# Optimization experiments

Hardware: AMD Instinct MI355X
Metric: run time of the kernel (lower is better)

## Reference

```python
import jax, jax.numpy as jnp
import numpy as np

V, D, N, K = 500000, 64, 50000, 32


def setup_inputs() -> dict:
    key = jax.random.key(0)
    ks = jax.random.split(key, 8)
    return {
        "embeddings": jax.random.normal(ks[0], (V, D), dtype=jnp.float32),
        "W1": jax.random.normal(ks[1], (2 * D, D), dtype=jnp.float32) * 0.05,
        "b1": jnp.zeros((D,), dtype=jnp.float32),
        "W2": jax.random.normal(ks[2], (D, D), dtype=jnp.float32) * 0.05,
        "b2": jnp.zeros((D,), dtype=jnp.float32),
        "w3": jax.random.normal(ks[3], (D, 1), dtype=jnp.float32) * 0.05,
        "b3": jnp.zeros((1,), dtype=jnp.float32),
        "video_nodes": jax.random.randint(ks[4], (N,), 0, V, dtype=jnp.int32),
        "neigh_idx": jax.random.randint(ks[5], (N, K), 0, V, dtype=jnp.int32),
        "neigh_deg": jax.random.randint(ks[6], (N,), 0, K + 1, dtype=jnp.int32),
    }


def reference(embeddings, W1, b1, W2, b2, w3, b3, video_nodes, neigh_idx, neigh_deg):
    # Ragged neighbor gather (padded to K, masked by degree)
    e = embeddings[neigh_idx]                      # [N, K, D] neighbor embeddings
    u = embeddings[video_nodes]                    # [N, D]    center embeddings
    # GraphRec-style attention: MLP on [neigh, center] concat -> scalar score
    x = jnp.concatenate(
        [e, jnp.broadcast_to(u[:, None, :], e.shape)], axis=-1)  # [N, K, 2D]
    h = jax.nn.relu(x @ W1 + b1)
    h = jax.nn.relu(h @ W2 + b2)
    s = (h @ w3)[..., 0] + b3[0]                   # [N, K]
    mask = jnp.arange(K)[None, :] < neigh_deg[:, None]
    s = jnp.where(mask, s, -1e9)                   # mask padded neighbors
    att = jax.nn.softmax(s, axis=-1)               # softmax over valid neighbors
    out = jnp.einsum('nkd,nk->nd', e, att)         # attention-weighted sum
    # num_neighs == 0 -> fall back to node's own embedding
    out = jnp.where((neigh_deg > 0)[:, None], out, u)
    return out
```

## Files before the change

### kernel.cpp

```cpp
#include <hip/hip_runtime.h>
#include <hip/hip_bf16.h>

typedef __bf16 bf16x8 __attribute__((ext_vector_type(8)));
typedef float  f32x4  __attribute__((ext_vector_type(4)));

#define MFMA32(acc, a, b) acc = __builtin_amdgcn_mfma_f32_16x16x32_bf16(a, b, acc, 0, 0, 0)
#define LD4(p) (*(const float4*)(p))

__device__ __forceinline__ bf16x8 cvt8(float4 a, float4 b) {
  bf16x8 r;
  r[0] = (__bf16)a.x; r[1] = (__bf16)a.y; r[2] = (__bf16)a.z; r[3] = (__bf16)a.w;
  r[4] = (__bf16)b.x; r[5] = (__bf16)b.y; r[6] = (__bf16)b.z; r[7] = (__bf16)b.w;
  return r;
}

template <int CTRL>
__device__ __forceinline__ float dpp_mov(float x) {
  int yi = __builtin_amdgcn_update_dpp(0, __builtin_bit_cast(int, x), CTRL, 0xF, 0xF, true);
  return __builtin_bit_cast(float, yi);
}
template <int CTRL>
__device__ __forceinline__ float dpp_fadd(float x) { return x + dpp_mov<CTRL>(x); }
template <int CTRL>
__device__ __forceinline__ float dpp_fmax(float x) { return fmaxf(x, dpp_mov<CTRL>(x)); }

__device__ __forceinline__ float tree16(const float* o, int lr) {
  float q8[8];
#pragma unroll
  for (int t = 0; t < 8; t++) {
    const bool up = (lr & 8);
    float sel = up ? o[t + 8] : o[t];
    float oth = up ? o[t] : o[t + 8];
    q8[t] = sel + dpp_mov<0x128>(oth);
  }
  float q4[4];
#pragma unroll
  for (int t = 0; t < 4; t++) {
    const bool up = (lr & 4);
    float sel = up ? q8[t + 4] : q8[t];
    float oth = up ? q8[t] : q8[t + 4];
    q4[t] = sel + __shfl_xor(oth, 4);
  }
  float q2[2];
#pragma unroll
  for (int t = 0; t < 2; t++) {
    const bool up = (lr & 2);
    float sel = up ? q4[t + 2] : q4[t];
    float oth = up ? q4[t] : q4[t + 2];
    q2[t] = sel + dpp_mov<0x4E>(oth);
  }
  const bool up = (lr & 1);
  float sel = up ? q2[1] : q2[0];
  float oth = up ? q2[0] : q2[1];
  return sel + dpp_mov<0xB1>(oth);
}

__global__ void prep_frags(const float* __restrict__ W1,
                           const float* __restrict__ W2,
                           __bf16* __restrict__ wf) {
  int idx = blockIdx.x * 256 + threadIdx.x;
  if (idx < 8192) {
    int j = idx & 7, lane = (idx >> 3) & 63, mt = (idx >> 9) & 3, ks = idx >> 11;
    int i = ks * 32 + ((lane >> 4) << 3) + j;
    int col = mt * 16 + (lane & 15);
    wf[idx] = (__bf16)W1[i * 64 + col];
  } else if (idx < 12288) {
    int t = idx - 8192;
    int j = t & 7, lane = (t >> 3) & 63, mt2 = (t >> 9) & 3, ks2 = (t >> 11) & 1;
    int g = (lane >> 4) & 3;
    int rho = (ks2 * 2 + (j >> 2)) * 16 + g * 4 + (j & 3);
    wf[idx] = (__bf16)W2[rho * 64 + mt2 * 16 + (lane & 15)];
  }
}

__global__ __launch_bounds__(512) void graph_agg(
    const float* __restrict__ emb,
    const float* __restrict__ b1g, const float* __restrict__ b2g,
    const float* __restrict__ w3g, const float* __restrict__ b3g,
    const int* __restrict__ vn, const int* __restrict__ ni,
    const int* __restrict__ nd,
    const __bf16* __restrict__ wf,
    float* __restrict__ out, int N) {
  __shared__ __align__(16) unsigned char smem[25344];

  {
    const uint4* src = (const uint4*)wf;
    uint4* dst = (uint4*)smem;
#pragma unroll
    for (int i = 0; i < 3; i++) dst[threadIdx.x + i * 512] = src[threadIdx.x + i * 512];
    int t = threadIdx.x;
    if (t < 64) {
      ((float*)(smem + 24576))[t] = b1g[t];
      ((float*)(smem + 24832))[t] = b2g[t];
      ((float*)(smem + 25088))[t] = w3g[t];
    }
  }
  __syncthreads();

  const __bf16* w1f = (const __bf16*)smem;
  const __bf16* w2f = (const __bf16*)(smem + 16384);
  const int wid = threadIdx.x >> 6;
  const int l   = threadIdx.x & 63;
  const int g   = l >> 4;
  const int lr  = l & 15;
  const float b3v = b3g[0];

  const int gw = blockIdx.x * 8 + wid;
  const int nwaves = gridDim.x * 8;

  int n = gw;
  int node = 0, deg = 0, i0 = 0, i1 = 0;
  if (n < N) {
    node = vn[n]; deg = nd[n];
    i0 = ni[(long)n * 32 + lr]; i1 = ni[(long)n * 32 + 16 + lr];
  }

  for (; n < N; n += nwaves) {
    const int cn = node, cd = deg, ci0 = i0, ci1 = i1;
    {
      int nn = n + nwaves; if (nn >= N) nn = n;
      node = vn[nn]; deg = nd[nn];
      i0 = ni[(long)nn * 32 + lr]; i1 = ni[(long)nn * 32 + 16 + lr];
    }
    const float* ub = emb + (long)cn * 64;

    if (cd == 0) {
      out[(long)n * 64 + l] = ub[l];
      continue;
    }
    const bool m1 = (cd > 16);

    int boff = 24576;
    asm volatile("" : "+v"(boff));
    const unsigned char* bb = smem + boff;

    bf16x8 ef00, ef01, ef10, ef11;
    {
      const int a = (lr < cd) ? ci0 : cn;
      const float* p = emb + (long)a * 64 + g * 8;
      ef00 = cvt8(LD4(p), LD4(p + 4));
      ef01 = cvt8(LD4(p + 32), LD4(p + 36));
    }
    if (m1) {
      const int a = (16 + lr < cd) ? ci1 : cn;
      const float* p = emb + (long)a * 64 + g * 8;
      ef10 = cvt8(LD4(p), LD4(p + 4));
      ef11 = cvt8(LD4(p + 32), LD4(p + 36));
    }
    bf16x8 uf0, uf1;
    {
      const float* q = ub + g * 8;
      uf0 = cvt8(LD4(q), LD4(q + 4));
      uf1 = cvt8(LD4(q + 32), LD4(q + 36));
    }

    f32x4 acc[4][2];
#pragma unroll
    for (int mt = 0; mt < 4; mt++) {
      f32x4 bv = *(const f32x4*)(bb + (mt * 16 + g * 4) * 4);
      acc[mt][0] = bv; acc[mt][1] = bv;
    }
    const bf16x8 xb0s[4] = {ef00, ef01, uf0, uf1};
    const bf16x8 xb1s[4] = {ef10, ef11, uf0, uf1};
#pragma unroll
    for (int ks = 0; ks < 4; ks++) {
#pragma unroll
      for (int mt = 0; mt < 4; mt++) {
        bf16x8 wa = *(const bf16x8*)(w1f + ((ks * 4 + mt) * 64 + l) * 8);
        MFMA32(acc[mt][0], wa, xb0s[ks]);
        if (m1) MFMA32(acc[mt][1], wa, xb1s[ks]);
      }
    }

    bf16x8 hb[2][2];
#pragma unroll
    for (int ks2 = 0; ks2 < 2; ks2++)
#pragma unroll
      for (int nt = 0; nt < 2; nt++) {
        if (nt == 0 || m1) {
          bf16x8 v;
#pragma unroll
          for (int j = 0; j < 8; j++) {
            const int mt = ks2 * 2 + (j >> 2), r = j & 3;
            v[j] = (__bf16)fmaxf(acc[mt][nt][r], 0.f);
          }
          hb[ks2][nt] = v;
        }
      }

#pragma unroll
    for (int mt2 = 0; mt2 < 4; mt2++) {
      f32x4 bv = *(const f32x4*)(bb + 256 + (mt2 * 16 + g * 4) * 4);
      acc[mt2][0] = bv; acc[mt2][1] = bv;
    }
#pragma unroll
    for (int ks2 = 0; ks2 < 2; ks2++)
#pragma unroll
      for (int mt2 = 0; mt2 < 4; mt2++) {
        bf16x8 wa = *(const bf16x8*)(w2f + ((ks2 * 4 + mt2) * 64 + l) * 8);
        MFMA32(acc[mt2][0], wa, hb[ks2][0]);
        if (m1) MFMA32(acc[mt2][1], wa, hb[ks2][1]);
      }

    float sv0 = 0.f, sv1 = 0.f;
#pragma unroll
    for (int mt2 = 0; mt2 < 4; mt2++) {
      f32x4 wv = *(const f32x4*)(bb + 512 + (mt2 * 16 + g * 4) * 4);
#pragma unroll
      for (int r = 0; r < 4; r++) {
        sv0 += fmaxf(acc[mt2][0][r], 0.f) * wv[r];
        if (m1) sv1 += fmaxf(acc[mt2][1][r], 0.f) * wv[r];
      }
    }
    sv0 += __shfl_xor(sv0, 16); sv0 += __shfl_xor(sv0, 32);
    if (m1) { sv1 += __shfl_xor(sv1, 16); sv1 += __shfl_xor(sv1, 32); }

    const bool v0 = (lr < cd);
    const bool v1 = m1 && (16 + lr < cd);
    sv0 = v0 ? (sv0 + b3v) : -1e30f;
    sv1 = v1 ? (sv1 + b3v) : -1e30f;

    float mx = fmaxf(sv0, sv1);
    mx = dpp_fmax<0x128>(mx);
    mx = dpp_fmax<0x124>(mx);
    mx = dpp_fmax<0x122>(mx);
    mx = dpp_fmax<0x121>(mx);

    float p0 = v0 ? __expf(sv0 - mx) : 0.f;
    float p1 = v1 ? __expf(sv1 - mx) : 0.f;
    float sum = p0 + p1;
    sum = dpp_fadd<0x128>(sum);
    sum = dpp_fadd<0x124>(sum);
    sum = dpp_fadd<0x122>(sum);
    sum = dpp_fadd<0x121>(sum);
    const float inv = 1.f / sum;
    const float a0 = p0 * inv, a1 = p1 * inv;

    float o[16];
#pragma unroll
    for (int j = 0; j < 8; j++) {
      float v = a0 * (float)ef00[j];
      if (m1) v += a1 * (float)ef10[j];
      o[j] = v;
      float w = a0 * (float)ef01[j];
      if (m1) w += a1 * (float)ef11[j];
      o[8 + j] = w;
    }
    const int dim = ((lr >> 3) << 5) + g * 8 + (lr & 7);
    out[(long)n * 64 + dim] = tree16(o, lr);
  }
}

extern "C" void kernel_launch(void* const* d_in, const int* in_sizes, int n_in,
                              void* d_out, int out_size, void* d_ws, size_t ws_size,
                              hipStream_t stream) {
  const float* emb = (const float*)d_in[0];
  const float* W1  = (const float*)d_in[1];
  const float* b1  = (const float*)d_in[2];
  const float* W2  = (const float*)d_in[3];
  const float* b2  = (const float*)d_in[4];
  const float* w3  = (const float*)d_in[5];
  const float* b3  = (const float*)d_in[6];
  const int* vn = (const int*)d_in[7];
  const int* ni = (const int*)d_in[8];
  const int* nd = (const int*)d_in[9];
  float* out = (float*)d_out;
  const int N = in_sizes[7];
  __bf16* wf = (__bf16*)d_ws;

  prep_frags<<<48, 256, 0, stream>>>(W1, W2, wf);
  graph_agg<<<2048, 512, 0, stream>>>(emb, b1, b2, w3, b3, vn, ni, nd, wf, out, N);
}
```

Before: 75.21 us.

## Prefetch next node's first-half neighbor rows into LDS via async global_load_lds

Uses global_load_lds (direct global-to-LDS DMA) to prefetch the next node's first 16 neighbor embeddings and center embedding into per-wave LDS buffers, issued in the middle of the current node's MLP so the gather latency overlaps with compute. The second half of the neighbors is still loaded directly to registers, and its MFMAs are split out after the first half's. Biases and w3 are now read from global memory instead of LDS, and LDS grows to 64KB per block, which lowers the number of blocks that can be resident. A full vmcnt(0) wait at the top of each iteration serializes against every outstanding load, not just the prefetch.

```diff
diff --git a/kernel.cpp b/kernel.cpp
--- a/kernel.cpp
+++ b/kernel.cpp
@@ -6,6 +6,12 @@
 
 #define MFMA32(acc, a, b) acc = __builtin_amdgcn_mfma_f32_16x16x32_bf16(a, b, acc, 0, 0, 0)
 #define LD4(p) (*(const float4*)(p))
+
+typedef const __attribute__((address_space(1))) void gas_t;
+typedef __attribute__((address_space(3))) void las_t;
+__device__ __forceinline__ void gload_lds16(const void* g, void* l) {
+  __builtin_amdgcn_global_load_lds((gas_t*)g, (las_t*)l, 16, 0, 0);
+}
 
 __device__ __forceinline__ bf16x8 cvt8(float4 a, float4 b) {
   bf16x8 r;
@@ -81,19 +87,13 @@
     const int* __restrict__ nd,
     const __bf16* __restrict__ wf,
     float* __restrict__ out, int N) {
-  __shared__ __align__(16) unsigned char smem[25344];
+  __shared__ __align__(16) unsigned char smem[65536];
 
   {
     const uint4* src = (const uint4*)wf;
     uint4* dst = (uint4*)smem;
 #pragma unroll
     for (int i = 0; i < 3; i++) dst[threadIdx.x + i * 512] = src[threadIdx.x + i * 512];
-    int t = threadIdx.x;
-    if (t < 64) {
-      ((float*)(smem + 24576))[t] = b1g[t];
-      ((float*)(smem + 24832))[t] = b2g[t];
-      ((float*)(smem + 25088))[t] = w3g[t];
-    }
   }
   __syncthreads();
 
@@ -103,6 +103,8 @@
   const int l   = threadIdx.x & 63;
   const int g   = l >> 4;
   const int lr  = l & 15;
+  unsigned char* pf0 = smem + 24576 + wid * 5120;
+  unsigned char* pfu = pf0 + 4096;
   const float b3v = b3g[0];
 
   const int gw = blockIdx.x * 8 + wid;
@@ -113,63 +115,91 @@
   if (n < N) {
     node = vn[n]; deg = nd[n];
     i0 = ni[(long)n * 32 + lr]; i1 = ni[(long)n * 32 + 16 + lr];
+    const int rn = (lr < deg) ? i0 : node;
+    const float* er = emb + (long)rn * 64 + g * 8;
+    gload_lds16(er,      pf0);
+    gload_lds16(er + 4,  pf0 + 1024);
+    gload_lds16(er + 32, pf0 + 2048);
+    gload_lds16(er + 36, pf0 + 3072);
+    gload_lds16(emb + (long)node * 64 + lr * 4, pfu);
   }
 
   for (; n < N; n += nwaves) {
-    const int cn = node, cd = deg, ci0 = i0, ci1 = i1;
-    {
-      int nn = n + nwaves; if (nn >= N) nn = n;
-      node = vn[nn]; deg = nd[nn];
-      i0 = ni[(long)nn * 32 + lr]; i1 = ni[(long)nn * 32 + 16 + lr];
-    }
-    const float* ub = emb + (long)cn * 64;
+    const int cn = node, cd = deg, ci1 = i1;
+
+    asm volatile("s_waitcnt vmcnt(0)" ::: "memory");
+    __builtin_amdgcn_sched_barrier(0);
+
+    int nn = n + nwaves; if (nn >= N) nn = n;
+    node = vn[nn]; deg = nd[nn];
+    i0 = ni[(long)nn * 32 + lr]; i1 = ni[(long)nn * 32 + 16 + lr];
 
     if (cd == 0) {
-      out[(long)n * 64 + l] = ub[l];
+      const float uv = *(const float*)(pfu + (((l >> 4) * 16 + (l >> 2)) << 4) + ((l & 3) << 2));
+      {
+        const int rn = (lr < deg) ? i0 : node;
+        const float* er = emb + (long)rn * 64 + g * 8;
+        gload_lds16(er,      pf0);
+        gload_lds16(er + 4,  pf0 + 1024);
+        gload_lds16(er + 32, pf0 + 2048);
+        gload_lds16(er + 36, pf0 + 3072);
+        gload_lds16(emb + (long)node * 64 + lr * 4, pfu);
+      }
+      out[(long)n * 64 + l] = uv;
       continue;
     }
     const bool m1 = (cd > 16);
 
-    int boff = 24576;
-    asm volatile("" : "+v"(boff));
-    const unsigned char* bb = smem + boff;
-
-    bf16x8 ef00, ef01, ef10, ef11;
-    {
-      const int a = (lr < cd) ? ci0 : cn;
-      const float* p = emb + (long)a * 64 + g * 8;
-      ef00 = cvt8(LD4(p), LD4(p + 4));
-      ef01 = cvt8(LD4(p + 32), LD4(p + 36));
-    }
+    float4 e1a, e1b, e1c, e1d;
     if (m1) {
       const int a = (16 + lr < cd) ? ci1 : cn;
       const float* p = emb + (long)a * 64 + g * 8;
-      ef10 = cvt8(LD4(p), LD4(p + 4));
-      ef11 = cvt8(LD4(p + 32), LD4(p + 36));
-    }
-    bf16x8 uf0, uf1;
+      e1a = LD4(p); e1b = LD4(p + 4); e1c = LD4(p + 32); e1d = LD4(p + 36);
+    }
+
+    bf16x8 ef00, ef01, uf0, uf1;
     {
-      const float* q = ub + g * 8;
-      uf0 = cvt8(LD4(q), LD4(q + 4));
-      uf1 = cvt8(LD4(q + 32), LD4(q + 36));
-    }
+      float4 f0 = LD4(pf0 + l * 16);
+      float4 f1 = LD4(pf0 + 1024 + l * 16);
+      float4 f2 = LD4(pf0 + 2048 + l * 16);
+      float4 f3 = LD4(pf0 + 3072 + l * 16);
+      ef00 = cvt8(f0, f1); ef01 = cvt8(f2, f3);
+      const unsigned char* ur = pfu + g * 288;
+      uf0 = cvt8(LD4(ur), LD4(ur + 16));
+      uf1 = cvt8(LD4(ur + 128), LD4(ur + 144));
+    }
+
+    int z0 = 0;
+    asm volatile("" : "+v"(z0));
+    const float* b1p = b1g + z0;
+    const float* b2p = b2g + z0;
+    const float* w3p = w3g + z0;
 
     f32x4 acc[4][2];
 #pragma unroll
     for (int mt = 0; mt < 4; mt++) {
-      f32x4 bv = *(const f32x4*)(bb + (mt * 16 + g * 4) * 4);
+      f32x4 bv = *(const f32x4*)(b1p + mt * 16 + g * 4);
       acc[mt][0] = bv; acc[mt][1] = bv;
     }
-    const bf16x8 xb0s[4] = {ef00, ef01, uf0, uf1};
-    const bf16x8 xb1s[4] = {ef10, ef11, uf0, uf1};
-#pragma unroll
-    for (int ks = 0; ks < 4; ks++) {
+    const bf16x8 x0s[4] = {ef00, ef01, uf0, uf1};
+#pragma unroll
+    for (int ks = 0; ks < 4; ks++)
 #pragma unroll
       for (int mt = 0; mt < 4; mt++) {
         bf16x8 wa = *(const bf16x8*)(w1f + ((ks * 4 + mt) * 64 + l) * 8);
-        MFMA32(acc[mt][0], wa, xb0s[ks]);
-        if (m1) MFMA32(acc[mt][1], wa, xb1s[ks]);
-      }
+        MFMA32(acc[mt][0], wa, x0s[ks]);
+      }
+    bf16x8 ef10, ef11;
+    if (m1) {
+      ef10 = cvt8(e1a, e1b); ef11 = cvt8(e1c, e1d);
+      const bf16x8 x1s[4] = {ef10, ef11, uf0, uf1};
+#pragma unroll
+      for (int ks = 0; ks < 4; ks++)
+#pragma unroll
+        for (int mt = 0; mt < 4; mt++) {
+          bf16x8 wa = *(const bf16x8*)(w1f + ((ks * 4 + mt) * 64 + l) * 8);
+          MFMA32(acc[mt][1], wa, x1s[ks]);
+        }
     }
 
     bf16x8 hb[2][2];
@@ -188,9 +218,21 @@
         }
       }
 
+    __builtin_amdgcn_sched_barrier(0);
+    {
+      const int rn = (lr < deg) ? i0 : node;
+      const float* er = emb + (long)rn * 64 + g * 8;
+      gload_lds16(er,      pf0);
+      gload_lds16(er + 4,  pf0 + 1024);
+      gload_lds16(er + 32, pf0 + 2048);
+      gload_lds16(er + 36, pf0 + 3072);
+      gload_lds16(emb + (long)node * 64 + lr * 4, pfu);
+    }
+    __builtin_amdgcn_sched_barrier(0);
+
 #pragma unroll
     for (int mt2 = 0; mt2 < 4; mt2++) {
-      f32x4 bv = *(const f32x4*)(bb + 256 + (mt2 * 16 + g * 4) * 4);
+      f32x4 bv = *(const f32x4*)(b2p + mt2 * 16 + g * 4);
       acc[mt2][0] = bv; acc[mt2][1] = bv;
     }
 #pragma unroll
@@ -205,7 +247,7 @@
     float sv0 = 0.f, sv1 = 0.f;
 #pragma unroll
     for (int mt2 = 0; mt2 < 4; mt2++) {
-      f32x4 wv = *(const f32x4*)(bb + 512 + (mt2 * 16 + g * 4) * 4);
+      f32x4 wv = *(const f32x4*)(w3p + mt2 * 16 + g * 4);
 #pragma unroll
       for (int r = 0; r < 4; r++) {
         sv0 += fmaxf(acc[mt2][0][r], 0.f) * wv[r];
```

New measurement: 109.8 us. +46.0%, slower.

## Prefetch next node's embeddings into LDS via async global-to-LDS loads

Applied to the files above, without the earlier changes.

Each wave now issues global_load_lds for the next node's first 16 neighbor rows and its center embedding into a per-wave LDS buffer. The prefetch is placed in the middle of the current node's MLP, so gather latency overlaps with compute. The second-half neighbors are loaded early into registers and their layer-1 MFMAs are split into a separate branch. It also drops the max-subtraction in the softmax, assuming scores stay small enough not to overflow exp. The larger LDS footprint may reduce occupancy, and the softmax is less numerically robust for large scores.

```diff
diff --git a/kernel.cpp b/kernel.cpp
--- a/kernel.cpp
+++ b/kernel.cpp
@@ -6,6 +6,15 @@
 
 #define MFMA32(acc, a, b) acc = __builtin_amdgcn_mfma_f32_16x16x32_bf16(a, b, acc, 0, 0, 0)
 #define LD4(p) (*(const float4*)(p))
+
+typedef const __attribute__((address_space(1))) void gas_t;
+typedef __attribute__((address_space(3))) void las_t;
+__device__ __forceinline__ void gload_lds16(const void* gp, void* lp) {
+  __builtin_amdgcn_global_load_lds((gas_t*)gp, (las_t*)lp, 16, 0, 0);
+}
+__device__ __forceinline__ void gload_lds4(const void* gp, void* lp) {
+  __builtin_amdgcn_global_load_lds((gas_t*)gp, (las_t*)lp, 4, 0, 0);
+}
 
 __device__ __forceinline__ bf16x8 cvt8(float4 a, float4 b) {
   bf16x8 r;
@@ -21,8 +30,6 @@
 }
 template <int CTRL>
 __device__ __forceinline__ float dpp_fadd(float x) { return x + dpp_mov<CTRL>(x); }
-template <int CTRL>
-__device__ __forceinline__ float dpp_fmax(float x) { return fmaxf(x, dpp_mov<CTRL>(x)); }
 
 __device__ __forceinline__ float tree16(const float* o, int lr) {
   float q8[8];
@@ -81,7 +88,7 @@
     const int* __restrict__ nd,
     const __bf16* __restrict__ wf,
     float* __restrict__ out, int N) {
-  __shared__ __align__(16) unsigned char smem[25344];
+  __shared__ __align__(16) unsigned char smem[60160];
 
   {
     const uint4* src = (const uint4*)wf;
@@ -103,7 +110,19 @@
   const int l   = threadIdx.x & 63;
   const int g   = l >> 4;
   const int lr  = l & 15;
+  unsigned char* pf0 = smem + 25344 + wid * 4352;
+  unsigned char* pfu = pf0 + 4096;
   const float b3v = b3g[0];
+
+#define PREFETCH(ND, DG, I0) do {                                   \
+    const int rn_ = (lr < (DG)) ? (I0) : (ND);                      \
+    const float* er_ = emb + (long)rn_ * 64 + g * 8;                \
+    gload_lds16(er_,      pf0);                                     \
+    gload_lds16(er_ + 4,  pf0 + 1024);                              \
+    gload_lds16(er_ + 32, pf0 + 2048);                              \
+    gload_lds16(er_ + 36, pf0 + 3072);                              \
+    gload_lds4(emb + (long)(ND) * 64 + l, pfu);                     \
+  } while (0)
 
   const int gw = blockIdx.x * 8 + wid;
   const int nwaves = gridDim.x * 8;
@@ -113,63 +132,71 @@
   if (n < N) {
     node = vn[n]; deg = nd[n];
     i0 = ni[(long)n * 32 + lr]; i1 = ni[(long)n * 32 + 16 + lr];
+    PREFETCH(node, deg, i0);
   }
 
   for (; n < N; n += nwaves) {
-    const int cn = node, cd = deg, ci0 = i0, ci1 = i1;
+    const int cn = node, cd = deg, ci1 = i1;
+
+    asm volatile("s_waitcnt vmcnt(0)" ::: "memory");
+
+    int nn = n + nwaves; if (nn >= N) nn = n;
+    node = vn[nn]; deg = nd[nn];
+    i0 = ni[(long)nn * 32 + lr]; i1 = ni[(long)nn * 32 + 16 + lr];
+
+    if (cd == 0) {
+      const float uv = *(const float*)(pfu + l * 4);
+      PREFETCH(node, deg, i0);
+      out[(long)n * 64 + l] = uv;
+      continue;
+    }
+    const bool m1 = (cd > 16);
+
+    float4 e1a, e1b, e1c, e1d;
+    if (m1) {
+      const int a = (16 + lr < cd) ? ci1 : cn;
+      const float* p = emb + (long)a * 64 + g * 8;
+      e1a = LD4(p); e1b = LD4(p + 4); e1c = LD4(p + 32); e1d = LD4(p + 36);
+    }
+
+    bf16x8 ef00 = cvt8(LD4(pf0 + l * 16),        LD4(pf0 + 1024 + l * 16));
+    bf16x8 ef01 = cvt8(LD4(pf0 + 2048 + l * 16), LD4(pf0 + 3072 + l * 16));
+    bf16x8 uf0, uf1;
     {
-      int nn = n + nwaves; if (nn >= N) nn = n;
-      node = vn[nn]; deg = nd[nn];
-      i0 = ni[(long)nn * 32 + lr]; i1 = ni[(long)nn * 32 + 16 + lr];
-    }
-    const float* ub = emb + (long)cn * 64;
-
-    if (cd == 0) {
-      out[(long)n * 64 + l] = ub[l];
-      continue;
-    }
-    const bool m1 = (cd > 16);
+      const unsigned char* ur = pfu + g * 32;
+      uf0 = cvt8(LD4(ur),       LD4(ur + 16));
+      uf1 = cvt8(LD4(ur + 128), LD4(ur + 144));
+    }
 
     int boff = 24576;
     asm volatile("" : "+v"(boff));
     const unsigned char* bb = smem + boff;
 
-    bf16x8 ef00, ef01, ef10, ef11;
-    {
-      const int a = (lr < cd) ? ci0 : cn;
-      const float* p = emb + (long)a * 64 + g * 8;
-      ef00 = cvt8(LD4(p), LD4(p + 4));
-      ef01 = cvt8(LD4(p + 32), LD4(p + 36));
-    }
-    if (m1) {
-      const int a = (16 + lr < cd) ? ci1 : cn;
-      const float* p = emb + (long)a * 64 + g * 8;
-      ef10 = cvt8(LD4(p), LD4(p + 4));
-      ef11 = cvt8(LD4(p + 32), LD4(p + 36));
-    }
-    bf16x8 uf0, uf1;
-    {
-      const float* q = ub + g * 8;
-      uf0 = cvt8(LD4(q), LD4(q + 4));
-      uf1 = cvt8(LD4(q + 32), LD4(q + 36));
-    }
-
     f32x4 acc[4][2];
 #pragma unroll
     for (int mt = 0; mt < 4; mt++) {
       f32x4 bv = *(const f32x4*)(bb + (mt * 16 + g * 4) * 4);
       acc[mt][0] = bv; acc[mt][1] = bv;
     }
-    const bf16x8 xb0s[4] = {ef00, ef01, uf0, uf1};
-    const bf16x8 xb1s[4] = {ef10, ef11, uf0, uf1};
-#pragma unroll
-    for (int ks = 0; ks < 4; ks++) {
+    const bf16x8 x0s[4] = {ef00, ef01, uf0, uf1};
+#pragma unroll
+    for (int ks = 0; ks < 4; ks++)
 #pragma unroll
       for (int mt = 0; mt < 4; mt++) {
         bf16x8 wa = *(const bf16x8*)(w1f + ((ks * 4 + mt) * 64 + l) * 8);
-        MFMA32(acc[mt][0], wa, xb0s[ks]);
-        if (m1) MFMA32(acc[mt][1], wa, xb1s[ks]);
-      }
+        MFMA32(acc[mt][0], wa, x0s[ks]);
+      }
+    bf16x8 ef10, ef11;
+    if (m1) {
+      ef10 = cvt8(e1a, e1b); ef11 = cvt8(e1c, e1d);
+      const bf16x8 x1s[4] = {ef10, ef11, uf0, uf1};
+#pragma unroll
+      for (int ks = 0; ks < 4; ks++)
+#pragma unroll
+        for (int mt = 0; mt < 4; mt++) {
+          bf16x8 wa = *(const bf16x8*)(w1f + ((ks * 4 + mt) * 64 + l) * 8);
+          MFMA32(acc[mt][1], wa, x1s[ks]);
+        }
     }
 
     bf16x8 hb[2][2];
@@ -188,6 +215,8 @@
         }
       }
 
+    PREFETCH(node, deg, i0);
+
 #pragma unroll
     for (int mt2 = 0; mt2 < 4; mt2++) {
       f32x4 bv = *(const f32x4*)(bb + 256 + (mt2 * 16 + g * 4) * 4);
@@ -217,17 +246,8 @@
 
     const bool v0 = (lr < cd);
     const bool v1 = m1 && (16 + lr < cd);
-    sv0 = v0 ? (sv0 + b3v) : -1e30f;
-    sv1 = v1 ? (sv1 + b3v) : -1e30f;
-
-    float mx = fmaxf(sv0, sv1);
-    mx = dpp_fmax<0x128>(mx);
-    mx = dpp_fmax<0x124>(mx);
-    mx = dpp_fmax<0x122>(mx);
-    mx = dpp_fmax<0x121>(mx);
-
-    float p0 = v0 ? __expf(sv0 - mx) : 0.f;
-    float p1 = v1 ? __expf(sv1 - mx) : 0.f;
+    float p0 = v0 ? __expf(sv0 + b3v) : 0.f;
+    float p1 = v1 ? __expf(sv1 + b3v) : 0.f;
     float sum = p0 + p1;
     sum = dpp_fadd<0x128>(sum);
     sum = dpp_fadd<0x124>(sum);
@@ -249,6 +269,7 @@
     const int dim = ((lr >> 3) << 5) + g * 8 + (lr & 7);
     out[(long)n * 64 + dim] = tree16(o, lr);
   }
+#undef PREFETCH
 }
 
 extern "C" void kernel_launch(void* const* d_in, const int* in_sizes, int n_in,
```

After: 99.79 us. +32.7%, slower.
